# Performance work log

Measured on AMD Instinct MI355X. Metric: run time of the kernel, lower is better.

## Reference

```python
import jax, jax.numpy as jnp
import numpy as np

B, S, E = 2, 2048, 2048
NH, NKV = 32, 8
HD = E // NH  # 64


def apply_rope(x, cos, sin):
    # x: [B, S, H, D]; cos/sin: [S, D]
    s, d = x.shape[1], x.shape[3]
    c = cos[:s, :d][None, :, None, :]
    sn = sin[:s, :d][None, :, None, :]
    x_rot = jnp.concatenate([-x[..., d // 2:], x[..., : d // 2]], axis=-1)
    return x * c + x_rot * sn


def setup_inputs() -> dict:
    key = jax.random.key(0)
    ks = jax.random.split(key, 6)
    x = jax.random.normal(ks[0], (B, S, E), dtype=jnp.float32)
    mask = jnp.ones((B, S), dtype=bool)
    # RoPE tables [S, HD]
    inv_freq = 1.0 / (10000.0 ** (jnp.arange(0, HD, 2, dtype=jnp.float32) / HD))
    freqs = jnp.arange(S, dtype=jnp.float32)[:, None] * inv_freq[None, :]
    emb = jnp.concatenate([freqs, freqs], axis=-1)  # [S, HD]
    cos = jnp.cos(emb)
    sin = jnp.sin(emb)
    sc = 1.0 / np.sqrt(E)
    Wq = jax.random.normal(ks[1], (E, E), dtype=jnp.float32) * sc
    Wk = jax.random.normal(ks[2], (NKV * HD, E), dtype=jnp.float32) * sc
    Wv = jax.random.normal(ks[3], (NKV * HD, E), dtype=jnp.float32) * sc
    Wo = jax.random.normal(ks[4], (E, E), dtype=jnp.float32) * sc
    return {"x": x, "mask": mask, "cos": cos, "sin": sin,
            "Wq": Wq, "Wk": Wk, "Wv": Wv, "Wo": Wo}


def reference(x, mask, cos, sin, Wq, Wk, Wv, Wo):
    b, s, e = x.shape
    scale = 1.0 / np.sqrt(HD)
    q = (x @ Wq.T).reshape(b, s, NH, HD)
    k = (x @ Wk.T).reshape(b, s, NKV, HD)
    v = (x @ Wv.T).reshape(b, s, NKV, HD)
    q = apply_rope(q, cos, sin)
    k = apply_rope(k, cos, sin)
    rep = NH // NKV
    # expand kv heads: [B,S,NKV,HD] -> [B,S,NH,HD]
    k = jnp.repeat(k, rep, axis=2)
    v = jnp.repeat(v, rep, axis=2)
    # [B,H,S,S]
    scores = jnp.einsum('bqhd,bkhd->bhqk', q, k) * scale
    causal = jnp.tril(jnp.ones((s, s), dtype=bool))
    combined = mask[:, None, None, :] & causal[None, None, :, :]
    scores = jnp.where(combined, scores, -jnp.inf)
    attn = jax.nn.softmax(scores, axis=-1)
    ctx = jnp.einsum('bhqk,bkhd->bqhd', attn, v).reshape(b, s, e)
    return ctx @ Wo.T
```

## Files before the change

kernel.cpp:

```cpp
#include <hip/hip_runtime.h>


typedef __attribute__((ext_vector_type(4))) float f32x4;
typedef __attribute__((ext_vector_type(16))) float f32x16;
typedef __attribute__((ext_vector_type(8))) __bf16 bf16x8;

#define SCL 0.18033688011112042f

__device__ __forceinline__ short f2bf(float f) {
  union { float f; unsigned u; } c; c.f = f;
  unsigned r = c.u + 0x7FFFu + ((c.u >> 16) & 1u);
  return (short)(r >> 16);
}

#define GLOAD16(g, l)                                                      \
  __builtin_amdgcn_global_load_lds(                                        \
      (const __attribute__((address_space(1))) unsigned int*)(g),          \
      (__attribute__((address_space(3))) unsigned int*)(l), 16, 0, 0)

__device__ __forceinline__ f32x4 mfma16(bf16x8 a, bf16x8 b, f32x4 c) {
  return __builtin_amdgcn_mfma_f32_16x16x32_bf16(a, b, c, 0, 0, 0);
}
__device__ __forceinline__ f32x16 mfma32(bf16x8 a, bf16x8 b, f32x16 c) {
  return __builtin_amdgcn_mfma_f32_32x32x16_bf16(a, b, c, 0, 0, 0);
}

__global__ void conv_bf16(const float* __restrict__ src, short* __restrict__ dst, int n) {
  int i = (blockIdx.x * blockDim.x + threadIdx.x) * 4;
  if (i >= n) return;
  float4 v = *(const float4*)(src + i);
  *(short4*)(dst + i) = make_short4(f2bf(v.x), f2bf(v.y), f2bf(v.z), f2bf(v.w));
}

template <int EPI>
__global__ __launch_bounds__(256, 2)
void gemm_bt(const short* __restrict__ A, const short* __restrict__ B,
             float* __restrict__ C, short* __restrict__ outK,
             short* __restrict__ outV, const float* __restrict__ cosT,
             const float* __restrict__ sinT, int M, int N, int K) {
  __shared__ short As[2][128 * 32];
  __shared__ short Bs[2][128 * 32];
  const int tid = threadIdx.x;
  const int lane = tid & 63;
  const int wm = (tid >> 6) >> 1;
  const int wn = (tid >> 6) & 1;
  const int m0 = blockIdx.x * 128;
  const int n0 = blockIdx.y * 128;
  const int kr = lane >> 4;
  const int lc = lane & 15;

  f32x4 acc[4][4] = {};

  const int lin0 = tid * 16;
  const int row0 = lin0 >> 6;
  const int slot0 = (lin0 >> 4) & 3;
  const int gs0 = slot0 ^ ((row0 >> 1) & 3);
  const int row1 = row0 + 64;
  const int gs1 = slot0 ^ ((row1 >> 1) & 3);
  const short* Ag0 = A + (size_t)(m0 + row0) * K + gs0 * 8;
  const short* Ag1 = A + (size_t)(m0 + row1) * K + gs1 * 8;
  const short* Bg0 = B + (size_t)(n0 + row0) * K + gs0 * 8;
  const short* Bg1 = B + (size_t)(n0 + row1) * K + gs1 * 8;
  const int dA0 = tid * 8;
  const int dA1 = tid * 8 + 2048;

  auto STAGE = [&](int k0, int buf) {
    GLOAD16(Ag0 + k0, &As[buf][dA0]);
    GLOAD16(Ag1 + k0, &As[buf][dA1]);
    GLOAD16(Bg0 + k0, &Bs[buf][dA0]);
    GLOAD16(Bg1 + k0, &Bs[buf][dA1]);
  };

  STAGE(0, 0);
  __syncthreads();
  int cur = 0;
  for (int k0 = 0; k0 < K; k0 += 32) {
    if (k0 + 32 < K) STAGE(k0 + 32, cur ^ 1);
    bf16x8 af[4], bfr[4];
#pragma unroll
    for (int i = 0; i < 4; ++i) {
      int r = wm * 64 + i * 16 + lc;
      af[i] = *(const bf16x8*)(&As[cur][r * 32 + ((kr ^ ((r >> 1) & 3)) << 3)]);
    }
#pragma unroll
    for (int j = 0; j < 4; ++j) {
      int r = wn * 64 + j * 16 + lc;
      bfr[j] = *(const bf16x8*)(&Bs[cur][r * 32 + ((kr ^ ((r >> 1) & 3)) << 3)]);
    }
#pragma unroll
    for (int i = 0; i < 4; ++i)
#pragma unroll
      for (int j = 0; j < 4; ++j)
        acc[i][j] = mfma16(af[i], bfr[j], acc[i][j]);
    __syncthreads();
    cur ^= 1;
  }

  if constexpr (EPI == 0) {
#pragma unroll
    for (int i = 0; i < 4; ++i) {
      int r0 = m0 + wm * 64 + i * 16 + kr * 4;
#pragma unroll
      for (int j = 0; j < 4; ++j) {
        int c = n0 + wn * 64 + j * 16 + lc;
#pragma unroll
        for (int ii = 0; ii < 4; ++ii)
          C[(size_t)(r0 + ii) * N + c] = acc[i][j][ii];
      }
    }
  } else if constexpr (EPI == 1) {
#pragma unroll
    for (int i = 0; i < 4; ++i) {
#pragma unroll
      for (int ii = 0; ii < 4; ++ii) {
        int r = m0 + wm * 64 + i * 16 + kr * 4 + ii;
        int s = r & 2047;
#pragma unroll
        for (int jp = 0; jp < 2; ++jp) {
          int d = jp * 16 + lc;
          float cs = cosT[s * 64 + d], sn = sinT[s * 64 + d];
          float x0 = acc[i][jp][ii], x1 = acc[i][jp + 2][ii];
          size_t base = (size_t)r * N + n0 + wn * 64;
          outK[base + jp * 16 + lc] = f2bf((x0 * cs - x1 * sn) * SCL);
          outK[base + (jp + 2) * 16 + lc] = f2bf((x1 * cs + x0 * sn) * SCL);
        }
      }
    }
  } else {
    if (n0 < 512) {
#pragma unroll
      for (int i = 0; i < 4; ++i) {
#pragma unroll
        for (int ii = 0; ii < 4; ++ii) {
          int r = m0 + wm * 64 + i * 16 + kr * 4 + ii;
          int s = r & 2047;
#pragma unroll
          for (int jp = 0; jp < 2; ++jp) {
            int d = jp * 16 + lc;
            float cs = cosT[s * 64 + d], sn = sinT[s * 64 + d];
            float x0 = acc[i][jp][ii], x1 = acc[i][jp + 2][ii];
            size_t base = (size_t)r * 512 + n0 + wn * 64;
            outK[base + jp * 16 + lc] = f2bf(x0 * cs - x1 * sn);
            outK[base + (jp + 2) * 16 + lc] = f2bf(x1 * cs + x0 * sn);
          }
        }
      }
    } else {
#pragma unroll
      for (int i = 0; i < 4; ++i) {
#pragma unroll
        for (int ii = 0; ii < 4; ++ii) {
          int r = m0 + wm * 64 + i * 16 + kr * 4 + ii;
#pragma unroll
          for (int j = 0; j < 4; ++j)
            outV[(size_t)r * 512 + (n0 - 512) + wn * 64 + j * 16 + lc] =
                f2bf(acc[i][j][ii]);
        }
      }
    }
  }
}

__global__ void transpose_v(const short* __restrict__ vtmp, short* __restrict__ vt) {
  __shared__ short Ls[64 * 66];
  int s0 = blockIdx.x * 64;
  int h = blockIdx.y;
  int b = blockIdx.z;
  int tid = threadIdx.x;
#pragma unroll
  for (int it = 0; it < 16; ++it) {
    int lin = it * 256 + tid;
    int r = lin >> 6, c = lin & 63;
    Ls[c * 66 + r] = vtmp[(size_t)(b * 2048 + s0 + r) * 512 + h * 64 + c];
  }
  __syncthreads();
#pragma unroll
  for (int it = 0; it < 16; ++it) {
    int lin = it * 256 + tid;
    int d = lin >> 6, c2 = lin & 63;
    vt[((size_t)((b * 8 + h) * 64 + d)) * 2048 + s0 + c2] = Ls[d * 66 + c2];
  }
}

__global__ __launch_bounds__(256, 2)
void attn(const short* __restrict__ Q, const short* __restrict__ Kk,
          const short* __restrict__ Vt, short* __restrict__ O) {
  const int qb = (int)gridDim.x - 1 - (int)blockIdx.x;
  const int h = blockIdx.y;
  const int b = blockIdx.z;
  const int kvh = h >> 2;
  const int tid = threadIdx.x;
  const int lane = tid & 63;
  const int w = tid >> 6;
  const int l5 = lane >> 5;
  const int lc5 = lane & 31;
  const int q0 = qb * 128;
  const int qrow = q0 + w * 32 + lc5;

  __shared__ short Ks[2][4096];
  __shared__ short Vs[2][4096];

  bf16x8 qreg[4];
  const short* qbase = Q + (size_t)(b * 2048 + qrow) * 2048 + h * 64 + l5 * 8;
#pragma unroll
  for (int s = 0; s < 4; ++s) qreg[s] = *(const bf16x8*)(qbase + s * 16);

  const short* kbs = Kk + (size_t)b * 2048 * 512 + kvh * 64;
  const short* vbs = Vt + (size_t)((b * 8 + kvh) * 64) * 2048;

  auto STAGE = [&](int kt, int buf) {
    GLOAD16(kbs + (size_t)(kt * 64 + lane) * 512 + w * 8, &Ks[buf][tid * 8]);
    GLOAD16(kbs + (size_t)(kt * 64 + lane) * 512 + (w + 4) * 8, &Ks[buf][tid * 8 + 2048]);
    GLOAD16(vbs + (size_t)lane * 2048 + kt * 64 + w * 8, &Vs[buf][tid * 8]);
    GLOAD16(vbs + (size_t)lane * 2048 + kt * 64 + (w + 4) * 8, &Vs[buf][tid * 8 + 2048]);
  };

  f32x16 oa0 = {}, oa1 = {};
  float mrow = -1e30f, lrow = 0.f;

  const int ktmax = (q0 + 127) >> 6;
  STAGE(0, 0);
  __syncthreads();
  int cur = 0;

  for (int kt = 0; kt <= ktmax; ++kt) {
    if (kt < ktmax) STAGE(kt + 1, cur ^ 1);

    if (kt * 64 <= q0 + w * 32 + 31) {
      f32x16 sa0 = {}, sa1 = {};
#pragma unroll
      for (int s = 0; s < 4; ++s) {
        const short* kp = &Ks[cur][(2 * s + l5) * 512 + lc5 * 8];
        sa0 = mfma32(*(const bf16x8*)kp, qreg[s], sa0);
        sa1 = mfma32(*(const bf16x8*)(kp + 256), qreg[s], sa1);
      }

      if (kt * 64 + 63 > q0 + w * 32) {
        const int kbase = kt * 64 + 4 * l5;
#pragma unroll
        for (int r = 0; r < 16; ++r) {
          int k = kbase + (r & 3) + 8 * (r >> 2);
          if (k > qrow) sa0[r] = -1e30f;
          if (k + 32 > qrow) sa1[r] = -1e30f;
        }
      }

      float mx = -1e30f;
#pragma unroll
      for (int r = 0; r < 16; ++r) mx = fmaxf(mx, fmaxf(sa0[r], sa1[r]));
      mx = fmaxf(mx, __shfl_xor(mx, 32));
      if (!__all(mx <= mrow + 8.f)) {
        float nm = fmaxf(mrow, mx);
        float rs = exp2f(mrow - nm);
        mrow = nm;
        lrow *= rs;
#pragma unroll
        for (int r = 0; r < 16; ++r) { oa0[r] *= rs; oa1[r] *= rs; }
      }
      float ps = 0.f;
#pragma unroll
      for (int r = 0; r < 16; ++r) {
        float p0 = exp2f(sa0[r] - mrow);
        float p1 = exp2f(sa1[r] - mrow);
        sa0[r] = p0; sa1[r] = p1;
        ps += p0 + p1;
      }
      ps += __shfl_xor(ps, 32);
      lrow += ps;

      unsigned pk0[8], pk1[8];
#pragma unroll
      for (int a = 0; a < 8; ++a) {
        asm("v_cvt_pk_bf16_f32 %0, %1, %2" : "=v"(pk0[a]) : "v"(sa0[2 * a]), "v"(sa0[2 * a + 1]));
        asm("v_cvt_pk_bf16_f32 %0, %1, %2" : "=v"(pk1[a]) : "v"(sa1[2 * a]), "v"(sa1[2 * a + 1]));
      }

#pragma unroll
      for (int s = 0; s < 4; ++s) {
        const int c = s & 1;
        unsigned x0 = (s < 2) ? pk0[4 * c + 0] : pk1[4 * c + 0];
        unsigned y0 = (s < 2) ? pk0[4 * c + 2] : pk1[4 * c + 2];
        unsigned x1 = (s < 2) ? pk0[4 * c + 1] : pk1[4 * c + 1];
        unsigned y1 = (s < 2) ? pk0[4 * c + 3] : pk1[4 * c + 3];
        asm("v_permlane32_swap_b32 %0, %1" : "+v"(x0), "+v"(y0));
        asm("v_permlane32_swap_b32 %0, %1" : "+v"(x1), "+v"(y1));
        union { unsigned u[4]; bf16x8 v; } pf;
        pf.u[0] = x0; pf.u[1] = x1; pf.u[2] = y0; pf.u[3] = y1;
        const short* vp = &Vs[cur][(2 * s + l5) * 512 + lc5 * 8];
        oa0 = mfma32(*(const bf16x8*)vp, pf.v, oa0);
        oa1 = mfma32(*(const bf16x8*)(vp + 256), pf.v, oa1);
      }
    }

    __syncthreads();
    cur ^= 1;
  }

  float inv = 1.0f / lrow;
  short* ob = O + (size_t)(b * 2048 + qrow) * 2048 + h * 64 + 4 * l5;
#pragma unroll
  for (int g = 0; g < 4; ++g) {
    *(short4*)(ob + 8 * g) =
        make_short4(f2bf(oa0[4 * g + 0] * inv), f2bf(oa0[4 * g + 1] * inv),
                    f2bf(oa0[4 * g + 2] * inv), f2bf(oa0[4 * g + 3] * inv));
    *(short4*)(ob + 32 + 8 * g) =
        make_short4(f2bf(oa1[4 * g + 0] * inv), f2bf(oa1[4 * g + 1] * inv),
                    f2bf(oa1[4 * g + 2] * inv), f2bf(oa1[4 * g + 3] * inv));
  }
}

extern "C" void kernel_launch(void* const* d_in, const int* in_sizes, int n_in,
                              void* d_out, int out_size, void* d_ws, size_t ws_size,
                              hipStream_t stream) {
  (void)in_sizes; (void)n_in; (void)out_size; (void)ws_size;
  const float* x    = (const float*)d_in[0];
  const float* cosT = (const float*)d_in[2];
  const float* sinT = (const float*)d_in[3];
  const float* Wq   = (const float*)d_in[4];
  const float* Wk   = (const float*)d_in[5];
  const float* Wv   = (const float*)d_in[6];
  const float* Wo   = (const float*)d_in[7];

  char* ws = (char*)d_ws;
  short* xb   = (short*)(ws + 0);
  short* Wqob = (short*)(ws + 16777216);
  short* Wkvb = (short*)(ws + 25165824);
  short* qr   = (short*)(ws + 29360128);
  short* kb   = (short*)(ws + 46137344);
  short* vtmp = (short*)(ws + 50331648);
  short* vt   = (short*)(ws + 54525952);
  short* ctx  = (short*)(ws + 58720256);

  conv_bf16<<<8192, 256, 0, stream>>>(x, xb, 8388608);
  conv_bf16<<<4096, 256, 0, stream>>>(Wq, Wqob, 4194304);
  conv_bf16<<<1024, 256, 0, stream>>>(Wk, Wkvb, 1048576);
  conv_bf16<<<1024, 256, 0, stream>>>(Wv, Wkvb + 1048576, 1048576);

  gemm_bt<1><<<dim3(32, 16), 256, 0, stream>>>(xb, Wqob, nullptr, qr, nullptr,
                                               cosT, sinT, 4096, 2048, 2048);
  gemm_bt<2><<<dim3(32, 8), 256, 0, stream>>>(xb, Wkvb, nullptr, kb, vtmp,
                                              cosT, sinT, 4096, 1024, 2048);

  transpose_v<<<dim3(32, 8, 2), 256, 0, stream>>>(vtmp, vt);
  conv_bf16<<<4096, 256, 0, stream>>>(Wo, Wqob, 4194304);

  attn<<<dim3(16, 32, 2), 256, 0, stream>>>(qr, kb, vt, ctx);

  gemm_bt<0><<<dim3(32, 16), 256, 0, stream>>>(ctx, Wqob, (float*)d_out, nullptr,
                                               nullptr, nullptr, nullptr,
                                               4096, 2048, 2048);
}
```

Before: 385.2 us.

## Triple-buffer GEMM and attention loads, pair causal query blocks, swizzle K/V LDS

```diff
diff --git a/kernel.cpp b/kernel.cpp
--- a/kernel.cpp
+++ b/kernel.cpp
@@ -17,6 +17,14 @@
   __builtin_amdgcn_global_load_lds(                                        \
       (const __attribute__((address_space(1))) unsigned int*)(g),          \
       (__attribute__((address_space(3))) unsigned int*)(l), 16, 0, 0)
+
+#define VM_WAIT4() asm volatile("s_waitcnt vmcnt(4)" ::: "memory")
+#define VM_WAIT0() asm volatile("s_waitcnt vmcnt(0)" ::: "memory")
+#define BARRIER()                        \
+  do {                                   \
+    __builtin_amdgcn_s_barrier();        \
+    asm volatile("" ::: "memory");       \
+  } while (0)
 
 __device__ __forceinline__ f32x4 mfma16(bf16x8 a, bf16x8 b, f32x4 c) {
   return __builtin_amdgcn_mfma_f32_16x16x32_bf16(a, b, c, 0, 0, 0);
@@ -38,8 +46,8 @@
              float* __restrict__ C, short* __restrict__ outK,
              short* __restrict__ outV, const float* __restrict__ cosT,
              const float* __restrict__ sinT, int M, int N, int K) {
-  __shared__ short As[2][128 * 32];
-  __shared__ short Bs[2][128 * 32];
+  __shared__ short As[3][128 * 32];
+  __shared__ short Bs[3][128 * 32];
   const int tid = threadIdx.x;
   const int lane = tid & 63;
   const int wm = (tid >> 6) >> 1;
@@ -72,10 +80,13 @@
   };
 
   STAGE(0, 0);
-  __syncthreads();
-  int cur = 0;
-  for (int k0 = 0; k0 < K; k0 += 32) {
-    if (k0 + 32 < K) STAGE(k0 + 32, cur ^ 1);
+  STAGE(32, 1);
+  const int nk = K >> 5;
+  for (int ik = 0; ik < nk; ++ik) {
+    if (ik + 1 < nk) VM_WAIT4(); else VM_WAIT0();
+    BARRIER();
+    if (ik + 2 < nk) STAGE((ik + 2) << 5, (ik + 2) % 3);
+    const int cur = ik % 3;
     bf16x8 af[4], bfr[4];
 #pragma unroll
     for (int i = 0; i < 4; ++i) {
@@ -87,13 +98,13 @@
       int r = wn * 64 + j * 16 + lc;
       bfr[j] = *(const bf16x8*)(&Bs[cur][r * 32 + ((kr ^ ((r >> 1) & 3)) << 3)]);
     }
+    __builtin_amdgcn_s_setprio(1);
 #pragma unroll
     for (int i = 0; i < 4; ++i)
 #pragma unroll
       for (int j = 0; j < 4; ++j)
         acc[i][j] = mfma16(af[i], bfr[j], acc[i][j]);
-    __syncthreads();
-    cur ^= 1;
+    __builtin_amdgcn_s_setprio(0);
   }
 
   if constexpr (EPI == 0) {
@@ -185,7 +196,7 @@
 __global__ __launch_bounds__(256, 2)
 void attn(const short* __restrict__ Q, const short* __restrict__ Kk,
           const short* __restrict__ Vt, short* __restrict__ O) {
-  const int qb = (int)gridDim.x - 1 - (int)blockIdx.x;
+  const int p = blockIdx.x;
   const int h = blockIdx.y;
   const int b = blockIdx.z;
   const int kvh = h >> 2;
@@ -194,118 +205,139 @@
   const int w = tid >> 6;
   const int l5 = lane >> 5;
   const int lc5 = lane & 31;
-  const int q0 = qb * 128;
-  const int qrow = q0 + w * 32 + lc5;
-
-  __shared__ short Ks[2][4096];
-  __shared__ short Vs[2][4096];
-
-  bf16x8 qreg[4];
-  const short* qbase = Q + (size_t)(b * 2048 + qrow) * 2048 + h * 64 + l5 * 8;
-#pragma unroll
-  for (int s = 0; s < 4; ++s) qreg[s] = *(const bf16x8*)(qbase + s * 16);
+
+  __shared__ short Ks[3][4096];
+  __shared__ short Vs[3][4096];
 
   const short* kbs = Kk + (size_t)b * 2048 * 512 + kvh * 64;
   const short* vbs = Vt + (size_t)((b * 8 + kvh) * 64) * 2048;
 
+  const int srow = tid >> 3;
+  const int sslot = tid & 7;
+  const int gs = sslot ^ (srow & 7);
+
   auto STAGE = [&](int kt, int buf) {
-    GLOAD16(kbs + (size_t)(kt * 64 + lane) * 512 + w * 8, &Ks[buf][tid * 8]);
-    GLOAD16(kbs + (size_t)(kt * 64 + lane) * 512 + (w + 4) * 8, &Ks[buf][tid * 8 + 2048]);
-    GLOAD16(vbs + (size_t)lane * 2048 + kt * 64 + w * 8, &Vs[buf][tid * 8]);
-    GLOAD16(vbs + (size_t)lane * 2048 + kt * 64 + (w + 4) * 8, &Vs[buf][tid * 8 + 2048]);
+    const short* kp = kbs + (size_t)(kt * 64 + srow) * 512 + gs * 8;
+    GLOAD16(kp, &Ks[buf][tid * 8]);
+    GLOAD16(kp + 32 * 512, &Ks[buf][tid * 8 + 2048]);
+    const short* vp = vbs + (size_t)srow * 2048 + kt * 64 + gs * 8;
+    GLOAD16(vp, &Vs[buf][tid * 8]);
+    GLOAD16(vp + 32 * 2048, &Vs[buf][tid * 8 + 2048]);
   };
 
-  f32x16 oa0 = {}, oa1 = {};
-  float mrow = -1e30f, lrow = 0.f;
-
-  const int ktmax = (q0 + 127) >> 6;
-  STAGE(0, 0);
-  __syncthreads();
-  int cur = 0;
-
-  for (int kt = 0; kt <= ktmax; ++kt) {
-    if (kt < ktmax) STAGE(kt + 1, cur ^ 1);
-
-    if (kt * 64 <= q0 + w * 32 + 31) {
-      f32x16 sa0 = {}, sa1 = {};
-#pragma unroll
-      for (int s = 0; s < 4; ++s) {
-        const short* kp = &Ks[cur][(2 * s + l5) * 512 + lc5 * 8];
-        sa0 = mfma32(*(const bf16x8*)kp, qreg[s], sa0);
-        sa1 = mfma32(*(const bf16x8*)(kp + 256), qreg[s], sa1);
-      }
-
-      if (kt * 64 + 63 > q0 + w * 32) {
-        const int kbase = kt * 64 + 4 * l5;
+  const int rx = lc5 & 7;
+
+#pragma unroll 1
+  for (int pass = 0; pass < 2; ++pass) {
+    const int qb = pass == 0 ? (15 - p) : p;
+    const int q0 = qb * 128;
+    const int qrow = q0 + w * 32 + lc5;
+    const int ktmax = 2 * qb + 1;
+
+    bf16x8 qreg[4];
+    const short* qbase = Q + (size_t)(b * 2048 + qrow) * 2048 + h * 64 + l5 * 8;
+#pragma unroll
+    for (int s = 0; s < 4; ++s) qreg[s] = *(const bf16x8*)(qbase + s * 16);
+
+    f32x16 oa0 = {}, oa1 = {};
+    float mrow = -1e30f, lrow = 0.f;
+
+    __syncthreads();
+    STAGE(0, 0);
+    STAGE(1, 1);
+
+    for (int kt = 0; kt <= ktmax; ++kt) {
+      if (kt < ktmax) VM_WAIT4(); else VM_WAIT0();
+      BARRIER();
+      if (kt + 2 <= ktmax) STAGE(kt + 2, (kt + 2) % 3);
+      const int cur = kt % 3;
+
+      if (kt * 64 <= q0 + w * 32 + 31) {
+        f32x16 sa0 = {}, sa1 = {};
+        __builtin_amdgcn_s_setprio(1);
+#pragma unroll
+        for (int s = 0; s < 4; ++s) {
+          const int so = (((2 * s + l5) ^ rx) << 3);
+          bf16x8 k0f = *(const bf16x8*)(&Ks[cur][lc5 * 64 + so]);
+          bf16x8 k1f = *(const bf16x8*)(&Ks[cur][(32 + lc5) * 64 + so]);
+          sa0 = mfma32(k0f, qreg[s], sa0);
+          sa1 = mfma32(k1f, qreg[s], sa1);
+        }
+        __builtin_amdgcn_s_setprio(0);
+
+        if (kt * 64 + 63 > q0 + w * 32) {
+          const int kbase = kt * 64 + 4 * l5;
+#pragma unroll
+          for (int r = 0; r < 16; ++r) {
+            int k = kbase + (r & 3) + 8 * (r >> 2);
+            if (k > qrow) sa0[r] = -1e30f;
+            if (k + 32 > qrow) sa1[r] = -1e30f;
+          }
+        }
+
+        float mx = -1e30f;
+#pragma unroll
+        for (int r = 0; r < 16; ++r) mx = fmaxf(mx, fmaxf(sa0[r], sa1[r]));
+        mx = fmaxf(mx, __shfl_xor(mx, 32));
+        if (!__all(mx <= mrow + 8.f)) {
+          float nm = fmaxf(mrow, mx);
+          float rs = exp2f(mrow - nm);
+          mrow = nm;
+          lrow *= rs;
+#pragma unroll
+          for (int r = 0; r < 16; ++r) { oa0[r] *= rs; oa1[r] *= rs; }
+        }
+        float ps = 0.f;
 #pragma unroll
         for (int r = 0; r < 16; ++r) {
-          int k = kbase + (r & 3) + 8 * (r >> 2);
-          if (k > qrow) sa0[r] = -1e30f;
-          if (k + 32 > qrow) sa1[r] = -1e30f;
-        }
-      }
-
-      float mx = -1e30f;
-#pragma unroll
-      for (int r = 0; r < 16; ++r) mx = fmaxf(mx, fmaxf(sa0[r], sa1[r]));
-      mx = fmaxf(mx, __shfl_xor(mx, 32));
-      if (!__all(mx <= mrow + 8.f)) {
-        float nm = fmaxf(mrow, mx);
-        float rs = exp2f(mrow - nm);
-        mrow = nm;
-        lrow *= rs;
-#pragma unroll
-        for (int r = 0; r < 16; ++r) { oa0[r] *= rs; oa1[r] *= rs; }
-      }
-      float ps = 0.f;
-#pragma unroll
-      for (int r = 0; r < 16; ++r) {
-        float p0 = exp2f(sa0[r] - mrow);
-        float p1 = exp2f(sa1[r] - mrow);
-        sa0[r] = p0; sa1[r] = p1;
-        ps += p0 + p1;
-      }
-      ps += __shfl_xor(ps, 32);
-      lrow += ps;
-
-      unsigned pk0[8], pk1[8];
-#pragma unroll
-      for (int a = 0; a < 8; ++a) {
-        asm("v_cvt_pk_bf16_f32 %0, %1, %2" : "=v"(pk0[a]) : "v"(sa0[2 * a]), "v"(sa0[2 * a + 1]));
-        asm("v_cvt_pk_bf16_f32 %0, %1, %2" : "=v"(pk1[a]) : "v"(sa1[2 * a]), "v"(sa1[2 * a + 1]));
-      }
-
-#pragma unroll
-      for (int s = 0; s < 4; ++s) {
-        const int c = s & 1;
-        unsigned x0 = (s < 2) ? pk0[4 * c + 0] : pk1[4 * c + 0];
-        unsigned y0 = (s < 2) ? pk0[4 * c + 2] : pk1[4 * c + 2];
-        unsigned x1 = (s < 2) ? pk0[4 * c + 1] : pk1[4 * c + 1];
-        unsigned y1 = (s < 2) ? pk0[4 * c + 3] : pk1[4 * c + 3];
-        asm("v_permlane32_swap_b32 %0, %1" : "+v"(x0), "+v"(y0));
-        asm("v_permlane32_swap_b32 %0, %1" : "+v"(x1), "+v"(y1));
-        union { unsigned u[4]; bf16x8 v; } pf;
-        pf.u[0] = x0; pf.u[1] = x1; pf.u[2] = y0; pf.u[3] = y1;
-        const short* vp = &Vs[cur][(2 * s + l5) * 512 + lc5 * 8];
-        oa0 = mfma32(*(const bf16x8*)vp, pf.v, oa0);
-        oa1 = mfma32(*(const bf16x8*)(vp + 256), pf.v, oa1);
-      }
-    }
-
-    __syncthreads();
-    cur ^= 1;
-  }
-
-  float inv = 1.0f / lrow;
-  short* ob = O + (size_t)(b * 2048 + qrow) * 2048 + h * 64 + 4 * l5;
-#pragma unroll
-  for (int g = 0; g < 4; ++g) {
-    *(short4*)(ob + 8 * g) =
-        make_short4(f2bf(oa0[4 * g + 0] * inv), f2bf(oa0[4 * g + 1] * inv),
-                    f2bf(oa0[4 * g + 2] * inv), f2bf(oa0[4 * g + 3] * inv));
-    *(short4*)(ob + 32 + 8 * g) =
-        make_short4(f2bf(oa1[4 * g + 0] * inv), f2bf(oa1[4 * g + 1] * inv),
-                    f2bf(oa1[4 * g + 2] * inv), f2bf(oa1[4 * g + 3] * inv));
+          float p0 = exp2f(sa0[r] - mrow);
+          float p1 = exp2f(sa1[r] - mrow);
+          sa0[r] = p0; sa1[r] = p1;
+          ps += p0 + p1;
+        }
+        ps += __shfl_xor(ps, 32);
+        lrow += ps;
+
+        unsigned pk0[8], pk1[8];
+#pragma unroll
+        for (int a = 0; a < 8; ++a) {
+          asm("v_cvt_pk_bf16_f32 %0, %1, %2" : "=v"(pk0[a]) : "v"(sa0[2 * a]), "v"(sa0[2 * a + 1]));
+          asm("v_cvt_pk_bf16_f32 %0, %1, %2" : "=v"(pk1[a]) : "v"(sa1[2 * a]), "v"(sa1[2 * a + 1]));
+        }
+
+        __builtin_amdgcn_s_setprio(1);
+#pragma unroll
+        for (int s = 0; s < 4; ++s) {
+          const int c = s & 1;
+          unsigned x0 = (s < 2) ? pk0[4 * c + 0] : pk1[4 * c + 0];
+          unsigned y0 = (s < 2) ? pk0[4 * c + 2] : pk1[4 * c + 2];
+          unsigned x1 = (s < 2) ? pk0[4 * c + 1] : pk1[4 * c + 1];
+          unsigned y1 = (s < 2) ? pk0[4 * c + 3] : pk1[4 * c + 3];
+          asm("v_permlane32_swap_b32 %0, %1" : "+v"(x0), "+v"(y0));
+          asm("v_permlane32_swap_b32 %0, %1" : "+v"(x1), "+v"(y1));
+          union { unsigned u[4]; bf16x8 v; } pf;
+          pf.u[0] = x0; pf.u[1] = x1; pf.u[2] = y0; pf.u[3] = y1;
+          const int so = (((2 * s + l5) ^ rx) << 3);
+          bf16x8 v0 = *(const bf16x8*)(&Vs[cur][lc5 * 64 + so]);
+          bf16x8 v1 = *(const bf16x8*)(&Vs[cur][(32 + lc5) * 64 + so]);
+          oa0 = mfma32(v0, pf.v, oa0);
+          oa1 = mfma32(v1, pf.v, oa1);
+        }
+        __builtin_amdgcn_s_setprio(0);
+      }
+    }
+
+    float inv = 1.0f / lrow;
+    short* ob = O + (size_t)(b * 2048 + qrow) * 2048 + h * 64 + 4 * l5;
+#pragma unroll
+    for (int g = 0; g < 4; ++g) {
+      *(short4*)(ob + 8 * g) =
+          make_short4(f2bf(oa0[4 * g + 0] * inv), f2bf(oa0[4 * g + 1] * inv),
+                      f2bf(oa0[4 * g + 2] * inv), f2bf(oa0[4 * g + 3] * inv));
+      *(short4*)(ob + 32 + 8 * g) =
+          make_short4(f2bf(oa1[4 * g + 0] * inv), f2bf(oa1[4 * g + 1] * inv),
+                      f2bf(oa1[4 * g + 2] * inv), f2bf(oa1[4 * g + 3] * inv));
+    }
   }
 }
 
@@ -344,7 +376,7 @@
   transpose_v<<<dim3(32, 8, 2), 256, 0, stream>>>(vtmp, vt);
   conv_bf16<<<4096, 256, 0, stream>>>(Wo, Wqob, 4194304);
 
-  attn<<<dim3(16, 32, 2), 256, 0, stream>>>(qr, kb, vt, ctx);
+  attn<<<dim3(8, 32, 2), 256, 0, stream>>>(qr, kb, vt, ctx);
 
   gemm_bt<0><<<dim3(32, 16), 256, 0, stream>>>(ctx, Wqob, (float*)d_out, nullptr,
                                                nullptr, nullptr, nullptr,
```

Measured after the change: 343.9 us. 1.12x faster.
